# Kernel tuning notes

Measured on AMD Instinct MI355X. Metric: run time of the kernel, lower is better.

## Reference

```python
import jax, jax.numpy as jnp
import numpy as np

L, B, E = 128, 16, 512
C_OUT = 64
KERNELS = [1, 3, 5, 7]
M = len(KERNELS) * C_OUT          # mlpdec_in = 256
OUT_SIZE = 256
SLOPE = 0.1


def setup_inputs() -> dict:
    key = jax.random.key(0)
    ks = jax.random.split(key, 32)
    s = 0.02
    d = {"x": jax.random.normal(ks[0], (L, B, E), dtype=jnp.float32)}
    # conv branches: weight (C_out, 1, k, E), bias (C_out,)
    for i, k in enumerate(KERNELS):
        d[f"cw{i}"] = jax.random.normal(ks[1 + 2 * i], (C_OUT, 1, k, E), dtype=jnp.float32) * s
        d[f"cb{i}"] = jnp.zeros((C_OUT,), dtype=jnp.float32)
    dims = [(C_OUT, 2 * M), (C_OUT, C_OUT), (C_OUT, C_OUT), (C_OUT, C_OUT)]
    for i, (o, inn) in enumerate(dims):
        d[f"mw{i}"] = jax.random.normal(ks[10 + 2 * i], (o, inn), dtype=jnp.float32) * s
        d[f"mb{i}"] = jnp.zeros((o,), dtype=jnp.float32)
    # mlp_layer: Linear(C->C), Linear(C->output_size)
    d["lw0"] = jax.random.normal(ks[20], (C_OUT, C_OUT), dtype=jnp.float32) * s
    d["lb0"] = jnp.zeros((C_OUT,), dtype=jnp.float32)
    d["lw1"] = jax.random.normal(ks[21], (OUT_SIZE, C_OUT), dtype=jnp.float32) * s
    d["lb1"] = jnp.zeros((OUT_SIZE,), dtype=jnp.float32)
    return d


def _lrelu(x):
    return jax.nn.leaky_relu(x, SLOPE)


def _conv_branch(xb, w, b):
    # xb: (B,1,L,E), w: (C,1,k,E) -> (B,C,L)
    k = w.shape[2]
    pad = (k - 1) // 2
    y = jax.lax.conv_general_dilated(
        xb, w, window_strides=(1, 1), padding=[(pad, pad), (0, 0)],
        dimension_numbers=("NCHW", "OIHW", "NCHW"))
    return _lrelu(y[..., 0] + b[None, :, None])


def reference(x, cw0, cb0, cw1, cb1, cw2, cb2, cw3, cb3,
              mw0, mb0, mw1, mb1, mw2, mb2, mw3, mb3,
              lw0, lb0, lw1, lb1):
    # x: (L,B,E) -> (B,1,L,E)
    xb = jnp.transpose(x, (1, 0, 2))[:, None, :, :]
    feats = jnp.concatenate([
        _conv_branch(xb, cw0, cb0), _conv_branch(xb, cw1, cb1),
        _conv_branch(xb, cw2, cb2), _conv_branch(xb, cw3, cb3)], axis=1)  # (B, 4C, L)
    f = jnp.transpose(feats, (2, 0, 1))  # (L, B, M)
    # pairwise: pair[i, j] = [f[j], f[i]]  -> (L, L, B, 2M)
    a = jnp.broadcast_to(f[None, :, :, :], (L, L, B, M))
    bpart = jnp.broadcast_to(f[:, None, :, :], (L, L, B, M))
    h = jnp.concatenate([a, bpart], axis=-1)
    for w, bb in ((mw0, mb0), (mw1, mb1), (mw2, mb2), (mw3, mb3)):
        h = _lrelu(h @ w.T + bb)
    h = h.sum(axis=0)  # (L, B, C)
    h = _lrelu(h @ lw0.T + lb0)
    return _lrelu(h @ lw1.T + lb1)  # (L, B, OUT_SIZE)
```

## Files before the change

kernel.cpp:

```cpp
#include <hip/hip_runtime.h>
#include <hip/hip_bf16.h>

#define SLOPE 0.1f
typedef unsigned short u16;
typedef unsigned int u32;
typedef __attribute__((ext_vector_type(8))) short short8;
typedef __attribute__((ext_vector_type(4))) float floatx4;

__device__ __forceinline__ float lrelu(float x) { return x > 0.0f ? x : SLOPE * x; }

__device__ __forceinline__ void split_rn(float x, u16* h, u16* l) {
    union { __hip_bfloat16 b; u16 u; } c1, c2;
    c1.b = __float2bfloat16(x);
    float hf = __bfloat162float(c1.b);
    c2.b = __float2bfloat16(x - hf);
    *h = c1.u; *l = c2.u;
}

__device__ __forceinline__ void split8(const float* __restrict__ p, short8& h8, short8& l8) {
    union { u16 us[8]; short8 v; } H, L;
    const float4 a = *(const float4*)p;
    const float4 b = *(const float4*)(p + 4);
    split_rn(a.x, &H.us[0], &L.us[0]); split_rn(a.y, &H.us[1], &L.us[1]);
    split_rn(a.z, &H.us[2], &L.us[2]); split_rn(a.w, &H.us[3], &L.us[3]);
    split_rn(b.x, &H.us[4], &L.us[4]); split_rn(b.y, &H.us[5], &L.us[5]);
    split_rn(b.z, &H.us[6], &L.us[6]); split_rn(b.w, &H.us[7], &L.us[7]);
    h8 = H.v; l8 = L.v;
}

__device__ __forceinline__ void pack2x2(float v0, float v1, u32& h, u32& l) {
    u32 a0 = __float_as_uint(v0), a1 = __float_as_uint(v1);
    h = __builtin_amdgcn_perm(a1, a0, 0x07060302u);
    float r0 = v0 - __uint_as_float(a0 & 0xFFFF0000u);
    float r1 = v1 - __uint_as_float(a1 & 0xFFFF0000u);
    l = __builtin_amdgcn_perm(__float_as_uint(r1), __float_as_uint(r0), 0x07060302u);
}

__device__ __forceinline__ short8 load_frag(const u16* p) {
    union { uint4 q; short8 s; } cv;
    cv.q = *(const uint4*)p;
    return cv.s;
}

__device__ __forceinline__ floatx4 mfma16(short8 a, short8 b, floatx4 c) {
    return __builtin_amdgcn_mfma_f32_16x16x32_bf16(a, b, c, 0, 0, 0);
}

__device__ __forceinline__ void prep_tail(int idx,
    const float* __restrict__ mw0, const float* __restrict__ mw1,
    const float* __restrict__ mw2, const float* __restrict__ mw3,
    const float* __restrict__ lw0, const float* __restrict__ lw1,
    u16* __restrict__ b2fh, u16* __restrict__ b2fl,
    u16* __restrict__ w3fh, u16* __restrict__ w3fl,
    float* __restrict__ lw0t, float* __restrict__ lw1t)
{
    if (idx < 32768) {
        const int j = idx & 7, lane = (idx >> 3) & 63;
        const int kc = (idx >> 9) & 7, nt = (idx >> 12) & 3, nh = idx >> 14;
        const int n = nh * 64 + nt * 16 + (lane & 15);
        const int k = kc * 32 + (lane >> 4) * 8 + j;
        const float4 s = *(const float4*)(mw0 + (n & 63) * 512 + (n >> 6) * 256 + k);
        u16 h[4], l[4];
        split_rn(s.x, &h[0], &l[0]); split_rn(s.y, &h[1], &l[1]);
        split_rn(s.z, &h[2], &l[2]); split_rn(s.w, &h[3], &l[3]);
        *(ushort4*)(b2fh + idx) = make_ushort4(h[0], h[1], h[2], h[3]);
        *(ushort4*)(b2fl + idx) = make_ushort4(l[0], l[1], l[2], l[3]);
        return;
    }
    idx -= 32768;
    if (idx < 12288) {
        const int j = idx & 7, lane = (idx >> 3) & 63;
        const int kc = (idx >> 9) & 1, mt = (idx >> 10) & 3, layer = idx >> 12;
        const float* mw = layer == 0 ? mw1 : layer == 1 ? mw2 : mw3;
        const int ch = mt * 16 + (lane & 15);
        const int k = kc * 32 + (lane >> 4) * 8 + j;
        const float4 s = *(const float4*)(mw + ch * 64 + k);
        u16 h[4], l[4];
        split_rn(s.x, &h[0], &l[0]); split_rn(s.y, &h[1], &l[1]);
        split_rn(s.z, &h[2], &l[2]); split_rn(s.w, &h[3], &l[3]);
        *(ushort4*)(w3fh + idx) = make_ushort4(h[0], h[1], h[2], h[3]);
        *(ushort4*)(w3fl + idx) = make_ushort4(l[0], l[1], l[2], l[3]);
        return;
    }
    idx -= 12288;
    if (idx < 4096) {
        const int k = idx >> 6, n = idx & 63;
        float4 o;
        o.x = lw0[(n + 0) * 64 + k]; o.y = lw0[(n + 1) * 64 + k];
        o.z = lw0[(n + 2) * 64 + k]; o.w = lw0[(n + 3) * 64 + k];
        *(float4*)(lw0t + idx) = o;
        return;
    }
    idx -= 4096;
    if (idx < 16384) {
        const int k = idx >> 8, n = idx & 255;
        float4 o;
        o.x = lw1[(n + 0) * 64 + k]; o.y = lw1[(n + 1) * 64 + k];
        o.z = lw1[(n + 2) * 64 + k]; o.w = lw1[(n + 3) * 64 + k];
        *(float4*)(lw1t + idx) = o;
        return;
    }
}

__global__ __launch_bounds__(512) void kA_conv(
    const float* __restrict__ x,
    const float* __restrict__ cw0, const float* __restrict__ cw1,
    const float* __restrict__ cw2, const float* __restrict__ cw3,
    const float* __restrict__ mw0, const float* __restrict__ mw1,
    const float* __restrict__ mw2, const float* __restrict__ mw3,
    const float* __restrict__ lw0, const float* __restrict__ lw1,
    u16* __restrict__ b2fh, u16* __restrict__ b2fl,
    u16* __restrict__ w3fh, u16* __restrict__ w3fl,
    float* __restrict__ lw0t, float* __restrict__ lw1t,
    float* __restrict__ Fp)
{
    __shared__ float P[8][16][72];

    const int t = threadIdx.x, lane = t & 63, w = t >> 6;
    const int slot = blockIdx.y;

    if (slot == 16) {
        const int gid = blockIdx.x * 512 + t;
        if (gid < 16384)
            prep_tail(gid * 4, mw0, mw1, mw2, mw3, lw0, lw1,
                      b2fh, b2fl, w3fh, w3fl, lw0t, lw1t);
        return;
    }

    const int rtp = blockIdx.x;
    int br, base;
    if (slot == 0)      { br = 0; base = 0; }
    else if (slot < 4)  { br = 1; base = 1; }
    else if (slot < 9)  { br = 2; base = 4; }
    else                { br = 3; base = 9; }
    const int dk = slot - base, ksz = 2 * br + 1;
    const int l15 = lane & 15, quad = lane >> 4;
    const float* cw = br == 0 ? cw0 : br == 1 ? cw1 : br == 2 ? cw2 : cw3;

    floatx4 acc[2][4];
    #pragma unroll
    for (int r = 0; r < 2; ++r)
        #pragma unroll
        for (int j = 0; j < 4; ++j) acc[r][j] = (floatx4)0.0f;

    #pragma unroll
    for (int kk = 0; kk < 2; ++kk) {
        const int kc = w * 2 + kk;
        const int e0 = kc * 32 + quad * 8;
        short8 bh[4], bl[4];
        #pragma unroll
        for (int nt = 0; nt < 4; ++nt) {
            const int c = nt * 16 + l15;
            split8(cw + (c * ksz + dk) * 512 + e0, bh[nt], bl[nt]);
        }
        #pragma unroll
        for (int r = 0; r < 2; ++r) {
            const int rts = rtp + r * 64 + dk - br;
            if (rts < 0 || rts >= 128) continue;
            short8 ah, al;
            split8(x + (rts * 16 + l15) * 512 + e0, ah, al);
            #pragma unroll
            for (int nt = 0; nt < 4; ++nt) {
                acc[r][nt] = mfma16(ah, bh[nt], acc[r][nt]);
                acc[r][nt] = mfma16(ah, bl[nt], acc[r][nt]);
                acc[r][nt] = mfma16(al, bh[nt], acc[r][nt]);
            }
        }
    }

    #pragma unroll
    for (int r = 0; r < 2; ++r) {
        #pragma unroll
        for (int nt = 0; nt < 4; ++nt)
            #pragma unroll
            for (int rr = 0; rr < 4; ++rr)
                P[w][quad * 4 + rr][nt * 16 + l15] = acc[r][nt][rr];
        __syncthreads();
        if (t < 256) {
            const int row = t >> 4, c4 = (t & 15) * 4;
            float4 o;
            #pragma unroll
            for (int i = 0; i < 4; ++i) {
                float val = P[0][row][c4 + i];
                #pragma unroll
                for (int ww = 1; ww < 8; ++ww) val += P[ww][row][c4 + i];
                (&o.x)[i] = val;
            }
            const int rowg = (rtp + r * 64) * 16 + row;
            *(float4*)(Fp + (slot * 2048 + rowg) * 64 + c4) = o;
        }
        __syncthreads();
    }
}

__global__ __launch_bounds__(256) void kB_uv(
    const float* __restrict__ Fp,
    const u16* __restrict__ b2fh, const u16* __restrict__ b2fl,
    const float* __restrict__ cb0, const float* __restrict__ cb1,
    const float* __restrict__ cb2, const float* __restrict__ cb3,
    const float* __restrict__ mb0,
    float* __restrict__ u, float* __restrict__ v_t)
{
    __shared__ float P[4][16][17];

    const int t = threadIdx.x, lane = t & 63, w = t >> 6;
    const int bid = blockIdx.x;
    const int rt = bid >> 3;
    const int nh = (bid >> 2) & 1;
    const int nt = bid & 3;
    const int l15 = lane & 15, quad = lane >> 4;

    floatx4 acc = (floatx4)0.0f;

    #pragma unroll
    for (int kk = 0; kk < 2; ++kk) {
        const int kc = w * 2 + kk;
        const int br2 = kc >> 1;
        const int base2 = br2 * br2, ksz2 = 2 * br2 + 1;
        const int cc0 = (kc & 1) * 32 + quad * 8;
        const int row = rt * 16 + l15;

        float s[8];
        #pragma unroll
        for (int j = 0; j < 8; ++j) s[j] = 0.0f;
        for (int d = 0; d < ksz2; ++d) {
            const float* pp = Fp + ((base2 + d) * 2048 + row) * 64 + cc0;
            const float4 q0 = *(const float4*)pp;
            const float4 q1 = *(const float4*)(pp + 4);
            s[0] += q0.x; s[1] += q0.y; s[2] += q0.z; s[3] += q0.w;
            s[4] += q1.x; s[5] += q1.y; s[6] += q1.z; s[7] += q1.w;
        }
        const float* cb = br2 == 0 ? cb0 : br2 == 1 ? cb1 : br2 == 2 ? cb2 : cb3;
        union { u16 us[8]; short8 v; } AH, AL;
        #pragma unroll
        for (int j = 0; j < 8; ++j) {
            const float val = lrelu(s[j] + cb[cc0 + j]);
            split_rn(val, &AH.us[j], &AL.us[j]);
        }
        const short8 ah = AH.v, al = AL.v;

        const int boff = (((nh * 4 + nt) * 8 + kc) * 64 + lane) * 8;
        const short8 bh = load_frag(b2fh + boff);
        const short8 bl = load_frag(b2fl + boff);
        acc = mfma16(ah, bh, acc);
        acc = mfma16(ah, bl, acc);
        acc = mfma16(al, bh, acc);
    }

    #pragma unroll
    for (int rr = 0; rr < 4; ++rr)
        P[w][quad * 4 + rr][l15] = acc[rr];
    __syncthreads();

    {
        const int row = t >> 4, c = t & 15;
        const float val = P[0][row][c] + P[1][row][c] + P[2][row][c] + P[3][row][c];
        const int rglob = rt * 16 + row;
        const int ch = nt * 16 + c;
        if (nh == 0) {
            u[rglob * 64 + ch] = val + mb0[ch];
        } else {
            const int i = rglob >> 4, b = rglob & 15;
            v_t[(b * 128 + i) * 64 + ch] = val;
        }
    }
}

__global__ __launch_bounds__(256, 4) void kC_pair(
    const float* __restrict__ u, const float* __restrict__ v_t,
    const u16* __restrict__ w3fh, const u16* __restrict__ w3fl,
    const float* __restrict__ mb1, const float* __restrict__ mb2,
    const float* __restrict__ mb3,
    const float* __restrict__ lw0t, const float* __restrict__ lb0,
    const float* __restrict__ lw1t, const float* __restrict__ lb1,
    float* __restrict__ out)
{
    __shared__ __align__(16) u16 Hh[128][72];
    __shared__ __align__(16) u16 Hl[128][72];
    __shared__ float Sp[4][64];
    __shared__ float Ss[64];
    __shared__ float T1[64];

    const int t = threadIdx.x, lane = t & 63, w = t >> 6;
    const int jb = blockIdx.x, b = jb & 15;
    const int l15 = lane & 15, quad = lane >> 4;
    const int i0 = w * 32;
    const int c4 = l15 * 4;

    const float4 uu = *(const float4*)(u + jb * 64 + c4);

    const float* vb = v_t + (b * 128 + i0) * 64;
    #pragma unroll
    for (int n = 0; n < 8; ++n) {
        const int idx = n * 64 + lane;
        const int il = idx >> 4;
        const float4 vv = *(const float4*)(vb + idx * 4);
        const float a0 = lrelu(vv.x + uu.x), a1 = lrelu(vv.y + uu.y);
        const float a2 = lrelu(vv.z + uu.z), a3 = lrelu(vv.w + uu.w);
        u32 h01, l01, h23, l23;
        pack2x2(a0, a1, h01, l01);
        pack2x2(a2, a3, h23, l23);
        *(uint2*)&Hh[i0 + il][c4] = make_uint2(h01, h23);
        *(uint2*)&Hl[i0 + il][c4] = make_uint2(l01, l23);
    }

    const float* mbp[3] = {mb1, mb2, mb3};
    for (int layer = 0; layer < 3; ++layer) {
        floatx4 acc[4][2];
        #pragma unroll
        for (int i = 0; i < 4; ++i)
            #pragma unroll
            for (int j = 0; j < 2; ++j) acc[i][j] = (floatx4)0.0f;

        #pragma unroll
        for (int kc = 0; kc < 2; ++kc) {
            short8 ah[4], al[4];
            #pragma unroll
            for (int mt = 0; mt < 4; ++mt) {
                const int aoff = (((layer * 4 + mt) * 2 + kc) * 64 + lane) * 8;
                ah[mt] = load_frag(w3fh + aoff);
                al[mt] = load_frag(w3fl + aoff);
            }
            const int k0 = kc * 32 + quad * 8;
            #pragma unroll
            for (int nt = 0; nt < 2; ++nt) {
                const short8 bh = load_frag(&Hh[i0 + nt * 16 + l15][k0]);
                const short8 bl = load_frag(&Hl[i0 + nt * 16 + l15][k0]);
                #pragma unroll
                for (int mt = 0; mt < 4; ++mt) {
                    acc[mt][nt] = mfma16(ah[mt], bh, acc[mt][nt]);
                    acc[mt][nt] = mfma16(ah[mt], bl, acc[mt][nt]);
                    acc[mt][nt] = mfma16(al[mt], bh, acc[mt][nt]);
                }
            }
        }

        if (layer < 2) {
            #pragma unroll
            for (int mt = 0; mt < 4; ++mt) {
                float bias[4];
                #pragma unroll
                for (int r = 0; r < 4; ++r) bias[r] = mbp[layer][mt * 16 + quad * 4 + r];
                #pragma unroll
                for (int nt = 0; nt < 2; ++nt) {
                    const int i = i0 + nt * 16 + l15;
                    const float v0 = lrelu(acc[mt][nt][0] + bias[0]);
                    const float v1 = lrelu(acc[mt][nt][1] + bias[1]);
                    const float v2 = lrelu(acc[mt][nt][2] + bias[2]);
                    const float v3 = lrelu(acc[mt][nt][3] + bias[3]);
                    u32 h01, l01, h23, l23;
                    pack2x2(v0, v1, h01, l01);
                    pack2x2(v2, v3, h23, l23);
                    *(uint2*)&Hh[i][mt * 16 + quad * 4] = make_uint2(h01, h23);
                    *(uint2*)&Hl[i][mt * 16 + quad * 4] = make_uint2(l01, l23);
                }
            }
        } else {
            #pragma unroll
            for (int mt = 0; mt < 4; ++mt) {
                float bias[4];
                #pragma unroll
                for (int r = 0; r < 4; ++r) bias[r] = mbp[2][mt * 16 + quad * 4 + r];
                float4 sv;
                #pragma unroll
                for (int r = 0; r < 4; ++r) {
                    float val = lrelu(acc[mt][0][r] + bias[r])
                              + lrelu(acc[mt][1][r] + bias[r]);
                    val += __shfl_xor(val, 1, 16);
                    val += __shfl_xor(val, 2, 16);
                    val += __shfl_xor(val, 4, 16);
                    val += __shfl_xor(val, 8, 16);
                    (&sv.x)[r] = val;
                }
                if (l15 == 0)
                    *(float4*)(&Sp[w][mt * 16 + quad * 4]) = sv;
            }
        }
    }

    __syncthreads();
    if (t < 64) Ss[t] = Sp[0][t] + Sp[1][t] + Sp[2][t] + Sp[3][t];
    __syncthreads();
    if (t < 64) {
        float a = lb0[t];
        #pragma unroll 8
        for (int k = 0; k < 64; ++k) a += Ss[k] * lw0t[k * 64 + t];
        T1[t] = lrelu(a);
    }
    __syncthreads();
    {
        float a = lb1[t];
        #pragma unroll 8
        for (int k = 0; k < 64; ++k) a += T1[k] * lw1t[k * 256 + t];
        out[jb * 256 + t] = lrelu(a);
    }
}

extern "C" void kernel_launch(void* const* d_in, const int* in_sizes, int n_in,
                              void* d_out, int out_size, void* d_ws, size_t ws_size,
                              hipStream_t stream)
{
    const float* x   = (const float*)d_in[0];
    const float* cw0 = (const float*)d_in[1];
    const float* cb0 = (const float*)d_in[2];
    const float* cw1 = (const float*)d_in[3];
    const float* cb1 = (const float*)d_in[4];
    const float* cw2 = (const float*)d_in[5];
    const float* cb2 = (const float*)d_in[6];
    const float* cw3 = (const float*)d_in[7];
    const float* cb3 = (const float*)d_in[8];
    const float* mw0 = (const float*)d_in[9];
    const float* mb0 = (const float*)d_in[10];
    const float* mw1 = (const float*)d_in[11];
    const float* mb1 = (const float*)d_in[12];
    const float* mw2 = (const float*)d_in[13];
    const float* mb2 = (const float*)d_in[14];
    const float* mw3 = (const float*)d_in[15];
    const float* mb3 = (const float*)d_in[16];
    const float* lw0 = (const float*)d_in[17];
    const float* lb0 = (const float*)d_in[18];
    const float* lw1 = (const float*)d_in[19];
    const float* lb1 = (const float*)d_in[20];
    float* out = (float*)d_out;

    char* base = (char*)d_ws;
    u16* b2fh   = (u16*)(base + 0);
    u16* b2fl   = (u16*)(base + 65536);
    u16* w3fh   = (u16*)(base + 131072);
    u16* w3fl   = (u16*)(base + 155648);
    float* lw0t = (float*)(base + 180224);
    float* lw1t = (float*)(base + 196608);
    float* Fp   = (float*)(base + 262144);
    float* u    = (float*)(base + 8650752);
    float* v_t  = (float*)(base + 9175040);

    hipLaunchKernelGGL(kA_conv, dim3(64, 17), dim3(512), 0, stream,
                       x, cw0, cw1, cw2, cw3, mw0, mw1, mw2, mw3, lw0, lw1,
                       b2fh, b2fl, w3fh, w3fl, lw0t, lw1t, Fp);
    hipLaunchKernelGGL(kB_uv, dim3(1024), dim3(256), 0, stream,
                       Fp, b2fh, b2fl, cb0, cb1, cb2, cb3, mb0, u, v_t);
    hipLaunchKernelGGL(kC_pair, dim3(2048), dim3(256), 0, stream,
                       u, v_t, w3fh, w3fl, mb1, mb2, mb3, lw0t, lb0, lw1t, lb1, out);
}
```

Before: 165.7 us.

## Drop low-bf16 activation term in pairwise MLP, keep split weights only

The pairwise kernel now stores activations as a single round-to-nearest bf16 value instead of a hi/lo split. This removes the Hl shared buffer and cuts the MFMA count per tile from three to two (weight hi and lo times activation hi). The smaller LDS footprint lets launch bounds rise to 8 blocks per CU, and the weight-fragment loads are interleaved with the MFMAs. The trade-off is lower accuracy in the activations, since the bf16 rounding error is no longer compensated.

```diff
diff --git a/kernel.cpp b/kernel.cpp
--- a/kernel.cpp
+++ b/kernel.cpp
@@ -28,12 +28,11 @@
     h8 = H.v; l8 = L.v;
 }
 
-__device__ __forceinline__ void pack2x2(float v0, float v1, u32& h, u32& l) {
-    u32 a0 = __float_as_uint(v0), a1 = __float_as_uint(v1);
-    h = __builtin_amdgcn_perm(a1, a0, 0x07060302u);
-    float r0 = v0 - __uint_as_float(a0 & 0xFFFF0000u);
-    float r1 = v1 - __uint_as_float(a1 & 0xFFFF0000u);
-    l = __builtin_amdgcn_perm(__float_as_uint(r1), __float_as_uint(r0), 0x07060302u);
+__device__ __forceinline__ u32 rn2(float v0, float v1) {
+    union { __hip_bfloat16 b; u16 u; } c0, c1;
+    c0.b = __float2bfloat16(v0);
+    c1.b = __float2bfloat16(v1);
+    return (u32)c0.u | ((u32)c1.u << 16);
 }
 
 __device__ __forceinline__ short8 load_frag(const u16* p) {
@@ -266,7 +265,7 @@
     }
 }
 
-__global__ __launch_bounds__(256, 4) void kC_pair(
+__global__ __launch_bounds__(256, 8) void k3_hi(
     const float* __restrict__ u, const float* __restrict__ v_t,
     const u16* __restrict__ w3fh, const u16* __restrict__ w3fl,
     const float* __restrict__ mb1, const float* __restrict__ mb2,
@@ -276,7 +275,6 @@
     float* __restrict__ out)
 {
     __shared__ __align__(16) u16 Hh[128][72];
-    __shared__ __align__(16) u16 Hl[128][72];
     __shared__ float Sp[4][64];
     __shared__ float Ss[64];
     __shared__ float T1[64];
@@ -297,11 +295,7 @@
         const float4 vv = *(const float4*)(vb + idx * 4);
         const float a0 = lrelu(vv.x + uu.x), a1 = lrelu(vv.y + uu.y);
         const float a2 = lrelu(vv.z + uu.z), a3 = lrelu(vv.w + uu.w);
-        u32 h01, l01, h23, l23;
-        pack2x2(a0, a1, h01, l01);
-        pack2x2(a2, a3, h23, l23);
-        *(uint2*)&Hh[i0 + il][c4] = make_uint2(h01, h23);
-        *(uint2*)&Hl[i0 + il][c4] = make_uint2(l01, l23);
+        *(uint2*)&Hh[i0 + il][c4] = make_uint2(rn2(a0, a1), rn2(a2, a3));
     }
 
     const float* mbp[3] = {mb1, mb2, mb3};
@@ -314,23 +308,20 @@
 
         #pragma unroll
         for (int kc = 0; kc < 2; ++kc) {
-            short8 ah[4], al[4];
+            const int k0 = kc * 32 + quad * 8;
+            short8 bh[2];
+            #pragma unroll
+            for (int nt = 0; nt < 2; ++nt)
+                bh[nt] = load_frag(&Hh[i0 + nt * 16 + l15][k0]);
             #pragma unroll
             for (int mt = 0; mt < 4; ++mt) {
                 const int aoff = (((layer * 4 + mt) * 2 + kc) * 64 + lane) * 8;
-                ah[mt] = load_frag(w3fh + aoff);
-                al[mt] = load_frag(w3fl + aoff);
-            }
-            const int k0 = kc * 32 + quad * 8;
-            #pragma unroll
-            for (int nt = 0; nt < 2; ++nt) {
-                const short8 bh = load_frag(&Hh[i0 + nt * 16 + l15][k0]);
-                const short8 bl = load_frag(&Hl[i0 + nt * 16 + l15][k0]);
-                #pragma unroll
-                for (int mt = 0; mt < 4; ++mt) {
-                    acc[mt][nt] = mfma16(ah[mt], bh, acc[mt][nt]);
-                    acc[mt][nt] = mfma16(ah[mt], bl, acc[mt][nt]);
-                    acc[mt][nt] = mfma16(al[mt], bh, acc[mt][nt]);
+                const short8 ah = load_frag(w3fh + aoff);
+                const short8 al = load_frag(w3fl + aoff);
+                #pragma unroll
+                for (int nt = 0; nt < 2; ++nt) {
+                    acc[mt][nt] = mfma16(ah, bh[nt], acc[mt][nt]);
+                    acc[mt][nt] = mfma16(al, bh[nt], acc[mt][nt]);
                 }
             }
         }
@@ -348,11 +339,8 @@
                     const float v1 = lrelu(acc[mt][nt][1] + bias[1]);
                     const float v2 = lrelu(acc[mt][nt][2] + bias[2]);
                     const float v3 = lrelu(acc[mt][nt][3] + bias[3]);
-                    u32 h01, l01, h23, l23;
-                    pack2x2(v0, v1, h01, l01);
-                    pack2x2(v2, v3, h23, l23);
-                    *(uint2*)&Hh[i][mt * 16 + quad * 4] = make_uint2(h01, h23);
-                    *(uint2*)&Hl[i][mt * 16 + quad * 4] = make_uint2(l01, l23);
+                    *(uint2*)&Hh[i][mt * 16 + quad * 4] =
+                        make_uint2(rn2(v0, v1), rn2(v2, v3));
                 }
             }
         } else {
@@ -439,6 +427,6 @@
                        b2fh, b2fl, w3fh, w3fl, lw0t, lw1t, Fp);
     hipLaunchKernelGGL(kB_uv, dim3(1024), dim3(256), 0, stream,
                        Fp, b2fh, b2fl, cb0, cb1, cb2, cb3, mb0, u, v_t);
-    hipLaunchKernelGGL(kC_pair, dim3(2048), dim3(256), 0, stream,
+    hipLaunchKernelGGL(k3_hi, dim3(2048), dim3(256), 0, stream,
                        u, v_t, w3fh, w3fl, mb1, mb2, mb3, lw0t, lb0, lw1t, lb1, out);
 }
```

After: 160.9 us. -2.9%, faster.
